# Kernel tuning notes

Measured on AMD Instinct MI355X. Metric: run time of the kernel, lower is better.

## Reference

```python
import jax, jax.numpy as jnp
import numpy as np

N_CLASSES = 16
B, N = 8, 2048
F = [128, 512, 1024]
K = [6, 5, 3]
M = [512, 128, 50]
IN_DIM = 22


def get_laplacian(x):
    # exp(-squared pairwise distance) adjacency, then normalized Laplacian I - D^-1/2 A D^-1/2
    inner = jnp.matmul(x, x.transpose(0, 2, 1))            # [B,N,N]
    sq = jnp.sum(x * x, axis=-1, keepdims=True)            # [B,N,1]
    adj = jnp.exp(-(sq - 2.0 * inner + sq.transpose(0, 2, 1)))
    dinv = 1.0 / jnp.sqrt(jnp.sum(adj, axis=-1))           # [B,N]
    Lnorm = dinv[:, :, None] * adj * dinv[:, None, :]
    return jnp.eye(x.shape[1], dtype=x.dtype) - Lnorm


def cheb_conv(x, L, W, b):
    # Chebyshev recursion: x0=x, x1=Lx, x_k = 2 L x_{k-1} - x_{k-2}; out = sum_k x_k @ W_k + b
    Kk = W.shape[0]
    x0 = x
    out = jnp.einsum('bni,io->bno', x0, W[0])
    if Kk > 1:
        x1 = jnp.matmul(L, x0)
        out = out + jnp.einsum('bni,io->bno', x1, W[1])
        for k in range(2, Kk):
            x2 = 2.0 * jnp.matmul(L, x1) - x0
            out = out + jnp.einsum('bni,io->bno', x2, W[k])
            x0, x1 = x1, x2
    return out + b


def setup_inputs() -> dict:
    key = jax.random.key(0)
    ks = jax.random.split(key, 24)
    d = {}
    d['x'] = jax.random.normal(ks[0], (B, N, 6), dtype=jnp.float32)
    d['cat'] = jax.random.randint(ks[1], (B, 1), 0, N_CLASSES)
    ins = [IN_DIM, F[0], F[1]]
    for i in range(3):
        s = 1.0 / np.sqrt(ins[i] * K[i])
        d[f'cheb_w{i}'] = jax.random.normal(ks[2 + i], (K[i], ins[i], F[i]), dtype=jnp.float32) * s
        d[f'cheb_b{i}'] = jnp.zeros((F[i],), dtype=jnp.float32)
    fc_ins = [F[-1], M[0] + M[0], M[1]]
    for i in range(3):
        s = 1.0 / np.sqrt(fc_ins[i])
        d[f'fc_w{i}'] = jax.random.normal(ks[6 + i], (fc_ins[i], M[i]), dtype=jnp.float32) * s
        d[f'fc_b{i}'] = jax.random.normal(ks[10 + i], (M[i],), dtype=jnp.float32) * s
    relus = F + M
    for i in range(6):
        d[f'br{i}'] = jnp.zeros((1, N, relus[i]), dtype=jnp.float32)
    return d


def reference(x, cat, cheb_w0, cheb_b0, cheb_w1, cheb_b1, cheb_w2, cheb_b2,
              fc_w0, fc_b0, fc_w1, fc_b1, fc_w2, fc_b2,
              br0, br1, br2, br3, br4, br5):
    L = jax.lax.stop_gradient(get_laplacian(x))  # torch.no_grad in original
    cat_oh = jax.nn.one_hot(cat, N_CLASSES, dtype=x.dtype)      # [B,1,16]
    cat_oh = jnp.tile(cat_oh, (1, N, 1))                         # [B,N,16]
    out = jnp.concatenate([x, cat_oh], axis=2)                   # [B,N,22]

    cheb_ws = [cheb_w0, cheb_w1, cheb_w2]
    cheb_bs = [cheb_b0, cheb_b1, cheb_b2]
    brs = [br0, br1, br2, br3, br4, br5]
    x1 = None
    for i in range(3):
        out = cheb_conv(out, L, cheb_ws[i], cheb_bs[i])
        out = jax.nn.relu(out + brs[i])  # dropout is identity in eval
        if i == 1:
            x1 = out

    fc_ws = [fc_w0, fc_w1, fc_w2]
    fc_bs = [fc_b0, fc_b1, fc_b2]
    for i in range(3):
        if i == 1:
            out = jnp.concatenate([out, x1], axis=2)
        out = jnp.einsum('bni,io->bno', out, fc_ws[i]) + fc_bs[i]
        out = jax.nn.relu(out + brs[i + 3])
    return out
```

## Files before the change

### kernel.cpp

```cpp
#include <hip/hip_runtime.h>
#include <stdint.h>

typedef __attribute__((ext_vector_type(8))) short short8;
typedef __attribute__((ext_vector_type(4))) float f32x4;

#define DEV __device__ __forceinline__

DEV ushort f2bf(float f){ uint32_t u = __float_as_uint(f); u += 0x7fffu + ((u >> 16) & 1u); return (ushort)(u >> 16); }
DEV float bf2f(ushort h){ return __uint_as_float(((uint32_t)h) << 16); }

template<int N> DEV void wvm(){
    asm volatile("s_waitcnt vmcnt(%0)" :: "i"(N) : "memory");
}


__global__ void wt_kernel(const float* __restrict__ src, ushort* __restrict__ dst,
                          int I, int O, int Opad, int blk, int srcF){
    int idx = blockIdx.x * 256 + threadIdx.x;
    if (idx >= Opad * I) return;
    int i = idx % I, o = idx / I;
    int k = i / blk, f = i % blk;
    ushort v = 0;
    if (o < O && f < srcF) v = f2bf(src[((long)k * srcF + f) * O + o]);
    dst[idx] = v;
}

__global__ void x0t_kernel(const float* __restrict__ x, const int* __restrict__ cat,
                           ushort* __restrict__ dst){
    int idx = blockIdx.x * 256 + threadIdx.x;
    int n = idx & 2047, f = (idx >> 11) & 31, b = idx >> 16;
    ushort v = 0;
    if (f < 6) v = f2bf(x[((long)b * 2048 + n) * 6 + f]);
    else if (f < 22) v = (cat[b] == f - 6) ? (ushort)0x3f80 : (ushort)0;
    dst[idx] = v;
}

__global__ void xt_kernel(const float* __restrict__ x, float* __restrict__ xT){
    int idx = blockIdx.x * 256 + threadIdx.x;
    if (idx >= 16384) return;
    int b = idx >> 11, n = idx & 2047;
    float* dst = xT + (long)b * 6 * 2048 + n;
#pragma unroll
    for (int d = 0; d < 6; d++) dst[d * 2048] = x[(long)idx * 6 + d];
}

__global__ __launch_bounds__(256) void dinv_kernel(const float* __restrict__ xT, float* __restrict__ dinv){
    int b = blockIdx.y;
    int wave = threadIdx.x >> 6, lane = threadIdx.x & 63;
    int i0 = blockIdx.x * 16 + wave * 4;
    const float* xtb = xT + (long)b * 6 * 2048;
    float xi[4][6];
#pragma unroll
    for (int ii = 0; ii < 4; ii++)
#pragma unroll
        for (int d = 0; d < 6; d++) xi[ii][d] = xtb[d * 2048 + i0 + ii];
    float s[4] = {0.f, 0.f, 0.f, 0.f};
#pragma unroll 2
    for (int jj = 0; jj < 32; jj++){
        int j = jj * 64 + lane;
        float xd[6];
#pragma unroll
        for (int d = 0; d < 6; d++) xd[d] = xtb[d * 2048 + j];
#pragma unroll
        for (int ii = 0; ii < 4; ii++){
            float a = 0.0f;
#pragma unroll
            for (int d = 0; d < 6; d++){ float t = xi[ii][d] - xd[d]; a += t * t; }
            s[ii] += __expf(-a);
        }
    }
#pragma unroll
    for (int ii = 0; ii < 4; ii++){
#pragma unroll
        for (int o = 32; o > 0; o >>= 1) s[ii] += __shfl_xor(s[ii], o);
    }
    if (lane == 0){
#pragma unroll
        for (int ii = 0; ii < 4; ii++) dinv[(b << 11) + i0 + ii] = rsqrtf(s[ii]);
    }
}

__global__ __launch_bounds__(256) void lap_kernel(const float* __restrict__ x, const float* __restrict__ dinv,
                                                  ushort* __restrict__ L){
    int b = blockIdx.z;
    int i0 = blockIdx.y * 32 + (threadIdx.x >> 6) * 8;
    int j0 = blockIdx.x * 512 + (threadIdx.x & 63) * 8;
    const float* xb = x + (long)b * 2048 * 6;
    const float* dv = dinv + (b << 11);
    f32x4 v[12];
    const f32x4* src = (const f32x4*)(xb + (long)j0 * 6);
#pragma unroll
    for (int c = 0; c < 12; c++) v[c] = src[c];
    const float* xj = (const float*)v;
    f32x4 dj0 = *(const f32x4*)(dv + j0);
    f32x4 dj1 = *(const f32x4*)(dv + j0 + 4);
    float dj[8] = {dj0[0], dj0[1], dj0[2], dj0[3], dj1[0], dj1[1], dj1[2], dj1[3]};
    ushort* out = L + ((long)b << 22) + (long)i0 * 2048 + j0;
#pragma unroll
    for (int ii = 0; ii < 8; ii++){
        const int i = i0 + ii;
        float xi[6];
#pragma unroll
        for (int d = 0; d < 6; d++) xi[d] = xb[i * 6 + d];
        const float di = dv[i];
        short8 o;
#pragma unroll
        for (int jj = 0; jj < 8; jj++){
            float a = 0.0f;
#pragma unroll
            for (int d = 0; d < 6; d++){ float t = xi[d] - xj[jj * 6 + d]; a += t * t; }
            float val = -di * dj[jj] * __expf(-a);
            if (i == j0 + jj) val += 1.0f;
            o[jj] = (short)f2bf(val);
        }
        *(short8*)(out + (long)ii * 2048) = o;
    }
}

__global__ void ts_kernel(const ushort* __restrict__ src, ushort* __restrict__ dst,
                          int F, int KF){
    int b = blockIdx.z;
    int i0 = blockIdx.y * 32;
    int k = i0 / F, f0 = i0 % F;
    int n0 = blockIdx.x * 64;
    __shared__ ushort t[32][66];
    const ushort* s = src + (((long)k * 8 + b) * F + f0) * 2048 + n0;
    int r = threadIdx.x >> 3, c8 = (threadIdx.x & 7) * 8;
    *(short8*)&t[r][c8] = *(const short8*)(s + (long)r * 2048 + c8);
    __syncthreads();
    int c = threadIdx.x >> 2, r8 = (threadIdx.x & 3) * 8;
    short8 v;
#pragma unroll
    for (int j = 0; j < 8; j++) v[j] = (short)t[r8 + j][c];
    *(short8*)(dst + ((long)b * 2048 + n0 + c) * KF + i0 + r8) = v;
}

__global__ void copy_x1_kernel(const ushort* __restrict__ src, ushort* __restrict__ dst){
    int idx = blockIdx.x * 256 + threadIdx.x;
    int r = idx >> 6, c = (idx & 63) * 8;
    *(short8*)(dst + (long)r * 1024 + 512 + c) = *(const short8*)(src + (long)r * 1536 + c);
}

template<int BM, int BN, int WR, int WC, int MODE>
__global__ __launch_bounds__(256) void gemm2(
    const ushort* __restrict__ A, int lda, long sA,
    const ushort* __restrict__ BT, int ldb, long sB,
    ushort* __restrict__ C, int ldc, long sC,
    int K,
    const ushort* __restrict__ Xp, long sX,
    const float* __restrict__ bias, const float* __restrict__ br, int brF,
    float* __restrict__ outF)
{
    constexpr int WM = BM / WR, WN = BN / WC, FM = WM / 16, FN = WN / 16;
    constexpr int ACH = BM / 16;
    constexpr int NCH = (BM + BN) / 16;
    __shared__ __align__(16) ushort As[BM * 32];
    __shared__ __align__(16) ushort Bs[BN * 32];
    const int tid = threadIdx.x, lane = tid & 63, wave = tid >> 6;
    const int wr = wave / WC, wc = wave % WC;
    const int bm0 = blockIdx.x * BM, bn0 = blockIdx.y * BN;
    const long z = blockIdx.z;
    A += z * sA; BT += z * sB;
    if (MODE != 4) C += z * sC;
    if (MODE == 1) Xp += z * sX;

    f32x4 acc[FM][FN];
#pragma unroll
    for (int m = 0; m < FM; m++)
#pragma unroll
        for (int n = 0; n < FN; n++) acc[m][n] = f32x4{0.f, 0.f, 0.f, 0.f};

    const int crow = lane >> 2;
    const int ccol = (lane & 3) * 8;

    for (int kt = 0; kt < K; kt += 32){
#pragma unroll
        for (int c = wave; c < NCH; c += 4){
            const ushort* gsrc;
            ushort* ldst;
            if (c < ACH){
                ldst = &As[c * 512];
                gsrc = A + (long)(bm0 + c * 16 + crow) * lda + kt + ccol;
            } else {
                ldst = &Bs[(c - ACH) * 512];
                gsrc = BT + (long)(bn0 + (c - ACH) * 16 + crow) * ldb + kt + ccol;
            }
            __builtin_amdgcn_global_load_lds(
                (const __attribute__((address_space(1))) void*)gsrc,
                (__attribute__((address_space(3))) void*)ldst, 16, 0, 0);
        }
        __syncthreads();
        const int kg = (lane >> 4) * 8;
        short8 af[FM], bfr[FN];
#pragma unroll
        for (int m = 0; m < FM; m++)
            af[m] = *(const short8*)&As[(wr * WM + m * 16 + (lane & 15)) * 32 + kg];
#pragma unroll
        for (int n = 0; n < FN; n++)
            bfr[n] = *(const short8*)&Bs[(wc * WN + n * 16 + (lane & 15)) * 32 + kg];
#pragma unroll
        for (int m = 0; m < FM; m++)
#pragma unroll
            for (int n = 0; n < FN; n++)
                acc[m][n] = __builtin_amdgcn_mfma_f32_16x16x32_bf16(af[m], bfr[n], acc[m][n], 0, 0, 0);
        __syncthreads();
    }

#pragma unroll
    for (int m = 0; m < FM; m++){
        const int r0 = bm0 + wr * WM + m * 16 + ((lane >> 4) << 2);
#pragma unroll
        for (int n = 0; n < FN; n++){
            const int col = bn0 + wc * WN + n * 16 + (lane & 15);
#pragma unroll
            for (int j = 0; j < 4; j++){
                const int r = r0 + j;
                float v = acc[m][n][j];
                if (MODE == 0){
                    C[(long)r * ldc + col] = f2bf(v);
                } else if (MODE == 1){
                    float p = bf2f(Xp[(long)r * ldc + col]);
                    C[(long)r * ldc + col] = f2bf(2.0f * v - p);
                } else if (MODE == 2){
                    float o = v + bias[r] + br[(long)col * brF + r];
                    C[(long)r * ldc + col] = f2bf(fmaxf(o, 0.0f));
                } else if (MODE == 3){
                    float o = v + bias[col] + br[(long)(r & 2047) * brF + col];
                    C[(long)r * ldc + col] = f2bf(fmaxf(o, 0.0f));
                } else {
                    if (col < 50){
                        float o = v + bias[col] + br[(long)(r & 2047) * 50 + col];
                        outF[(long)r * 50 + col] = fmaxf(o, 0.0f);
                    }
                }
            }
        }
    }
}

template<int BM, int BN, int MODE>
__global__ __launch_bounds__(256) void gmv(
    const ushort* __restrict__ A, int lda, long sA,
    const ushort* __restrict__ BT, int ldb, long sB,
    ushort* __restrict__ C, int ldc, long sC,
    int K,
    const ushort* __restrict__ Xp, long sX)
{
    constexpr int WM = BM / 2, WN = BN / 2, FM = WM / 16, FN = WN / 16;
    constexpr int ACH = BM / 8;
    constexpr int NCH = (BM + BN) / 8;
    constexpr int LPW = NCH / 4;
    static_assert(NCH % 4 == 0, "uniform loads per wave");
    __shared__ __align__(16) ushort lds[3 * (BM + BN) * 64];
    const int tid = threadIdx.x, lane = tid & 63, wave = tid >> 6;
    const int wr = wave >> 1, wc = wave & 1;
    const long z = blockIdx.x;
    const int bm0 = blockIdx.y * BM, bn0 = blockIdx.z * BN;
    A += z * sA; BT += z * sB; C += z * sC;
    if (MODE == 1) Xp += z * sX;
    const int NT = K >> 6;

    const int srow = lane >> 3;
    const int kloc = ((lane & 7) ^ srow) * 8;

    auto stage = [&](int u, int sel){
        ushort* dst0 = lds + sel * (BM + BN) * 64;
#pragma unroll
        for (int i = 0; i < LPW; i++){
            int c = i * 4 + wave;
            ushort* ldst = dst0 + c * 512;
            const ushort* src;
            if (c < ACH) src = A + (long)(bm0 + c * 8 + srow) * lda + u * 64 + kloc;
            else         src = BT + (long)(bn0 + (c - ACH) * 8 + srow) * ldb + u * 64 + kloc;
            __builtin_amdgcn_global_load_lds(
                (const __attribute__((address_space(1))) void*)src,
                (__attribute__((address_space(3))) void*)ldst, 16, 0, 0);
        }
    };

    f32x4 acc[FM][FN];
#pragma unroll
    for (int m = 0; m < FM; m++)
#pragma unroll
        for (int n = 0; n < FN; n++) acc[m][n] = f32x4{0.f, 0.f, 0.f, 0.f};

    stage(0, 0);
    if (NT > 1) stage(1, 1);

    int sel = 0;
    for (int u = 0; u < NT; u++){
        if (u + 1 < NT) wvm<LPW>(); else wvm<0>();
        __builtin_amdgcn_sched_barrier(0);
        __builtin_amdgcn_s_barrier();
        __builtin_amdgcn_sched_barrier(0);
        const char* base = (const char*)lds + sel * (BM + BN) * 128;
        const int hi = (lane >> 4) << 4;
        short8 af[FM], bfr[FN];
#pragma unroll
        for (int h = 0; h < 2; h++){
            const int kb = h * 64 + hi;
#pragma unroll
            for (int m = 0; m < FM; m++){
                int row = wr * WM + m * 16 + (lane & 15);
                af[m] = *(const short8*)(base + row * 128 + (kb ^ ((row & 7) << 4)));
            }
#pragma unroll
            for (int n = 0; n < FN; n++){
                int row = BM + wc * WN + n * 16 + (lane & 15);
                bfr[n] = *(const short8*)(base + row * 128 + (kb ^ ((row & 7) << 4)));
            }
            __builtin_amdgcn_s_setprio(1);
#pragma unroll
            for (int m = 0; m < FM; m++)
#pragma unroll
                for (int n = 0; n < FN; n++)
                    acc[m][n] = __builtin_amdgcn_mfma_f32_16x16x32_bf16(af[m], bfr[n], acc[m][n], 0, 0, 0);
            __builtin_amdgcn_s_setprio(0);
        }
        if (u + 2 < NT) stage(u + 2, (u + 2) % 3);
        sel = (sel == 2) ? 0 : sel + 1;
    }

#pragma unroll
    for (int m = 0; m < FM; m++){
        const int r0 = bm0 + wr * WM + m * 16 + ((lane >> 4) << 2);
#pragma unroll
        for (int n = 0; n < FN; n++){
            const int col = bn0 + wc * WN + n * 16 + (lane & 15);
#pragma unroll
            for (int j = 0; j < 4; j++){
                const int r = r0 + j;
                float v = acc[m][n][j];
                if (MODE == 0){
                    C[(long)r * ldc + col] = f2bf(v);
                } else {
                    float p = bf2f(Xp[(long)r * ldc + col]);
                    C[(long)r * ldc + col] = f2bf(2.0f * v - p);
                }
            }
        }
    }
}

template<int MODE, int SWZ>
__global__ __launch_bounds__(512) void gemm8(
    const ushort* __restrict__ A, int lda, long sA,
    const ushort* __restrict__ BT, int ldb, long sB,
    ushort* __restrict__ C, int ldc, long sC,
    int K,
    const ushort* __restrict__ Xp, long sX,
    const float* __restrict__ bias, const float* __restrict__ br, int brF)
{
    __shared__ __align__(16) ushort lds[73728];
    const int tid = threadIdx.x, lane = tid & 63, wave = tid >> 6;
    const int wr = wave >> 1, wc = wave & 1;
    const int bm0 = (SWZ ? blockIdx.y : blockIdx.x) * 256;
    const int bn0 = (SWZ ? blockIdx.z : blockIdx.y) * 128;
    const long z = SWZ ? blockIdx.x : blockIdx.z;
    A += z * sA; BT += z * sB; C += z * sC;
    if (MODE == 1) Xp += z * sX;
    const int NT = K >> 6;

    const int srow = lane >> 3;
    const int kloc = ((lane & 7) ^ srow) * 8;

    auto stageA = [&](int u, int sel){
        ushort* dst0 = lds + sel * 24576;
        const ushort* src = A + (long)u * 64 + kloc;
#pragma unroll
        for (int c = 0; c < 4; c++){
            int row = (c * 8 + wave) * 8 + srow;
            __builtin_amdgcn_global_load_lds(
                (const __attribute__((address_space(1))) void*)(src + (long)(bm0 + row) * lda),
                (__attribute__((address_space(3))) void*)(dst0 + (c * 8 + wave) * 512), 16, 0, 0);
        }
    };
    auto stageB = [&](int u, int sel){
        ushort* dst0 = lds + sel * 24576 + 16384;
        const ushort* src = BT + (long)u * 64 + kloc;
#pragma unroll
        for (int c = 0; c < 2; c++){
            int row = (c * 8 + wave) * 8 + srow;
            __builtin_amdgcn_global_load_lds(
                (const __attribute__((address_space(1))) void*)(src + (long)(bn0 + row) * ldb),
                (__attribute__((address_space(3))) void*)(dst0 + (c * 8 + wave) * 512), 16, 0, 0);
        }
    };

    f32x4 acc[4][4];
#pragma unroll
    for (int m = 0; m < 4; m++)
#pragma unroll
        for (int n = 0; n < 4; n++) acc[m][n] = f32x4{0.f, 0.f, 0.f, 0.f};

    stageA(0, 0); stageB(0, 0);
    stageA(1, 1); stageB(1, 1);
    asm volatile("s_waitcnt vmcnt(6)" ::: "memory");
    __builtin_amdgcn_sched_barrier(0);
    __builtin_amdgcn_s_barrier();
    __builtin_amdgcn_sched_barrier(0);

    int bsel = 0;
    for (int u = 0; u < NT; u++){
        const char* Ab = (const char*)lds + bsel * 49152;
        const char* Bb = Ab + 32768;
        const int stsel = bsel ? bsel - 1 : 2;
        const bool do_stage = (u + 2 < NT);
        const int hi = (lane >> 4) << 4;
        short8 af[4], bf[4];
#pragma unroll
        for (int m = 0; m < 4; m++){
            int row = wr * 64 + m * 16 + (lane & 15);
            af[m] = *(const short8*)(Ab + row * 128 + (hi ^ ((row & 7) << 4)));
        }
#pragma unroll
        for (int n = 0; n < 4; n++){
            int row = wc * 64 + n * 16 + (lane & 15);
            bf[n] = *(const short8*)(Bb + row * 128 + (hi ^ ((row & 7) << 4)));
        }
        if (do_stage) stageA(u + 2, stsel);
        __builtin_amdgcn_sched_barrier(0);
        __builtin_amdgcn_s_barrier();
        __builtin_amdgcn_s_setprio(1);
#pragma unroll
        for (int m = 0; m < 4; m++)
#pragma unroll
            for (int n = 0; n < 4; n++)
                acc[m][n] = __builtin_amdgcn_mfma_f32_16x16x32_bf16(af[m], bf[n], acc[m][n], 0, 0, 0);
        __builtin_amdgcn_s_setprio(0);
        __builtin_amdgcn_sched_barrier(0);
        __builtin_amdgcn_s_barrier();
        __builtin_amdgcn_sched_barrier(0);
#pragma unroll
        for (int m = 0; m < 4; m++){
            int row = wr * 64 + m * 16 + (lane & 15);
            af[m] = *(const short8*)(Ab + row * 128 + ((64 + hi) ^ ((row & 7) << 4)));
        }
#pragma unroll
        for (int n = 0; n < 4; n++){
            int row = wc * 64 + n * 16 + (lane & 15);
            bf[n] = *(const short8*)(Bb + row * 128 + ((64 + hi) ^ ((row & 7) << 4)));
        }
        if (do_stage) stageB(u + 2, stsel);
        __builtin_amdgcn_sched_barrier(0);
        __builtin_amdgcn_s_barrier();
        __builtin_amdgcn_s_setprio(1);
#pragma unroll
        for (int m = 0; m < 4; m++)
#pragma unroll
            for (int n = 0; n < 4; n++)
                acc[m][n] = __builtin_amdgcn_mfma_f32_16x16x32_bf16(af[m], bf[n], acc[m][n], 0, 0, 0);
        __builtin_amdgcn_s_setprio(0);
        if (do_stage){ asm volatile("s_waitcnt vmcnt(6)" ::: "memory"); }
        else        { asm volatile("s_waitcnt vmcnt(0)" ::: "memory"); }
        __builtin_amdgcn_sched_barrier(0);
        __builtin_amdgcn_s_barrier();
        __builtin_amdgcn_sched_barrier(0);
        bsel = (bsel == 2) ? 0 : bsel + 1;
    }

#pragma unroll
    for (int m = 0; m < 4; m++){
        const int r0 = bm0 + wr * 64 + m * 16 + ((lane >> 4) << 2);
#pragma unroll
        for (int n = 0; n < 4; n++){
            const int col = bn0 + wc * 64 + n * 16 + (lane & 15);
#pragma unroll
            for (int j = 0; j < 4; j++){
                const int r = r0 + j;
                float v = acc[m][n][j];
                if (MODE == 0){
                    C[(long)r * ldc + col] = f2bf(v);
                } else if (MODE == 1){
                    float p = bf2f(Xp[(long)r * ldc + col]);
                    C[(long)r * ldc + col] = f2bf(2.0f * v - p);
                } else if (MODE == 2){
                    float o = v + bias[r] + br[(long)col * brF + r];
                    C[(long)r * ldc + col] = f2bf(fmaxf(o, 0.0f));
                } else {
                    float o = v + bias[col] + br[(long)(r & 2047) * brF + col];
                    C[(long)r * ldc + col] = f2bf(fmaxf(o, 0.0f));
                }
            }
        }
    }
}


extern "C" void kernel_launch(void* const* d_in, const int* in_sizes, int n_in,
                              void* d_out, int out_size, void* d_ws, size_t ws_size,
                              hipStream_t stream){
    const float* x   = (const float*)d_in[0];
    const int*   cat = (const int*)d_in[1];
    const float* cw0 = (const float*)d_in[2];
    const float* cb0 = (const float*)d_in[3];
    const float* cw1 = (const float*)d_in[4];
    const float* cb1 = (const float*)d_in[5];
    const float* cw2 = (const float*)d_in[6];
    const float* cb2 = (const float*)d_in[7];
    const float* fw0 = (const float*)d_in[8];
    const float* fb0 = (const float*)d_in[9];
    const float* fw1 = (const float*)d_in[10];
    const float* fb1 = (const float*)d_in[11];
    const float* fw2 = (const float*)d_in[12];
    const float* fb2 = (const float*)d_in[13];
    const float* br0 = (const float*)d_in[14];
    const float* br1 = (const float*)d_in[15];
    const float* br2 = (const float*)d_in[16];
    const float* br3 = (const float*)d_in[17];
    const float* br4 = (const float*)d_in[18];
    const float* br5 = (const float*)d_in[19];
    float* out = (float*)d_out;
    (void)in_sizes; (void)n_in; (void)out_size; (void)ws_size;

    char* ws = (char*)d_ws;
    long off = 0;
    auto take = [&](long bytes){ char* p = ws + off; off += (bytes + 255) & ~255L; return p; };
    ushort* Lb   = (ushort*)take(8L * 2048 * 2048 * 2);
    float*  din  = (float*) take(8L * 2048 * 4);
    float*  XT   = (float*) take(8L * 6 * 2048 * 4);
    ushort* W0T  = (ushort*)take(128L * 192 * 2);
    ushort* W1T  = (ushort*)take(512L * 640 * 2);
    ushort* W2T  = (ushort*)take(1024L * 1536 * 2);
    ushort* WF0T = (ushort*)take(512L * 1024 * 2);
    ushort* WF1T = (ushort*)take(128L * 1024 * 2);
    ushort* WF2T = (ushort*)take(64L * 128 * 2);
    ushort* ST0T = (ushort*)take(6L * 8 * 32 * 2048 * 2);
    ushort* S0   = (ushort*)take(16384L * 192 * 2);
    ushort* ST1T = (ushort*)take(5L * 8 * 128 * 2048 * 2);
    ushort* S1   = (ushort*)take(16384L * 640 * 2);
    ushort* ST2T = (ushort*)take(3L * 8 * 512 * 2048 * 2);
    ushort* S2   = (ushort*)take(16384L * 1536 * 2);
    ushort* X3 = Lb;
    ushort* CC = ST2T;
    ushort* H5 = ST0T;

    const long NN = 2048L * 2048;
    const long s0k = 8L * 32 * 2048,  s0b = 32L * 2048;
    const long s1k = 8L * 128 * 2048, s1b = 128L * 2048;
    const long s2k = 8L * 512 * 2048, s2b = 512L * 2048;

    wt_kernel<<<(128 * 192 + 255) / 256, 256, 0, stream>>>(cw0, W0T, 192, 128, 128, 32, 22);
    wt_kernel<<<(512 * 640 + 255) / 256, 256, 0, stream>>>(cw1, W1T, 640, 512, 512, 128, 128);
    wt_kernel<<<(1024 * 1536 + 255) / 256, 256, 0, stream>>>(cw2, W2T, 1536, 1024, 1024, 512, 512);
    wt_kernel<<<(512 * 1024 + 255) / 256, 256, 0, stream>>>(fw0, WF0T, 1024, 512, 512, 1024, 1024);
    wt_kernel<<<(128 * 1024 + 255) / 256, 256, 0, stream>>>(fw1, WF1T, 1024, 128, 128, 1024, 1024);
    wt_kernel<<<(64 * 128 + 255) / 256, 256, 0, stream>>>(fw2, WF2T, 128, 50, 64, 128, 128);

    x0t_kernel<<<2048, 256, 0, stream>>>(x, cat, ST0T);
    xt_kernel<<<64, 256, 0, stream>>>(x, XT);
    dinv_kernel<<<dim3(128, 8), 256, 0, stream>>>(XT, din);
    lap_kernel<<<dim3(4, 64, 8), 256, 0, stream>>>(x, din, Lb);

    gmv<32, 32, 0><<<dim3(8, 1, 64), 256, 0, stream>>>(
        ST0T, 2048, s0b, Lb, 2048, NN, ST0T + s0k, 2048, s0b, 2048, nullptr, 0);
    for (int k = 2; k < 6; k++)
        gmv<32, 32, 1><<<dim3(8, 1, 64), 256, 0, stream>>>(
            ST0T + (k - 1) * s0k, 2048, s0b, Lb, 2048, NN, ST0T + k * s0k, 2048, s0b, 2048,
            ST0T + (k - 2) * s0k, s0b);
    ts_kernel<<<dim3(32, 6, 8), 256, 0, stream>>>(ST0T, S0, 32, 192);
    gemm2<64, 128, 2, 2, 2><<<dim3(2, 16, 8), 256, 0, stream>>>(
        W0T, 192, 0, S0, 192, 2048L * 192, ST1T, 2048, s1b, 192, nullptr, 0, cb0, br0, 128, nullptr);

    gmv<128, 32, 0><<<dim3(8, 1, 64), 256, 0, stream>>>(
        ST1T, 2048, s1b, Lb, 2048, NN, ST1T + s1k, 2048, s1b, 2048, nullptr, 0);
    for (int k = 2; k < 5; k++)
        gmv<128, 32, 1><<<dim3(8, 1, 64), 256, 0, stream>>>(
            ST1T + (k - 1) * s1k, 2048, s1b, Lb, 2048, NN, ST1T + k * s1k, 2048, s1b, 2048,
            ST1T + (k - 2) * s1k, s1b);
    ts_kernel<<<dim3(32, 20, 8), 256, 0, stream>>>(ST1T, S1, 128, 640);
    gemm8<2, 1><<<dim3(8, 2, 16), 512, 0, stream>>>(
        W1T, 640, 0, S1, 640, 2048L * 640, ST2T, 2048, s2b, 640, nullptr, 0, cb1, br1, 512);

    gemm8<0, 1><<<dim3(8, 2, 16), 512, 0, stream>>>(
        ST2T, 2048, s2b, Lb, 2048, NN, ST2T + s2k, 2048, s2b, 2048, nullptr, 0, nullptr, nullptr, 0);
    gemm8<1, 1><<<dim3(8, 2, 16), 512, 0, stream>>>(
        ST2T + s2k, 2048, s2b, Lb, 2048, NN, ST2T + 2 * s2k, 2048, s2b, 2048,
        ST2T, s2b, nullptr, nullptr, 0);
    ts_kernel<<<dim3(32, 48, 8), 256, 0, stream>>>(ST2T, S2, 512, 1536);
    gemm8<3, 0><<<dim3(64, 8, 1), 512, 0, stream>>>(
        S2, 1536, 0, W2T, 1536, 0, X3, 1024, 0, 1536, nullptr, 0, cb2, br2, 1024);

    gemm8<3, 0><<<dim3(64, 4, 1), 512, 0, stream>>>(
        X3, 1024, 0, WF0T, 1024, 0, CC, 1024, 0, 1024, nullptr, 0, fb0, br3, 512);
    copy_x1_kernel<<<4096, 256, 0, stream>>>(S2, CC);
    gemm2<128, 64, 2, 2, 3><<<dim3(128, 2, 1), 256, 0, stream>>>(
        CC, 1024, 0, WF1T, 1024, 0, H5, 128, 0, 1024, nullptr, 0, fb1, br4, 128, nullptr);
    gemm2<128, 64, 2, 2, 4><<<dim3(128, 1, 1), 256, 0, stream>>>(
        H5, 128, 0, WF2T, 128, 0, nullptr, 0, 0, 128, nullptr, 0, fb2, br5, 50, out);
}
```

Measured before the change: 462.5 us.

## Replace 256x128 triple-buffered GEMM with 128x128 double-buffered 256-thread kernel

The large bf16 MFMA GEMM kernel now uses 128x128 block tiles with 4 waves instead of 256x128 tiles with 8 waves. The LDS staging drops from a triple buffer to a double buffer, with A and B loaded by one combined routine. Each iteration now waits for all outstanding loads before its closing barrier. All launches double their block count in M, which gives more blocks per CU and smaller LDS use. The cost is less data reuse per block and a shallower prefetch pipeline that exposes more memory latency.

```diff
diff --git a/kernel.cpp b/kernel.cpp
--- a/kernel.cpp
+++ b/kernel.cpp
@@ -343,7 +343,7 @@
 }
 
 template<int MODE, int SWZ>
-__global__ __launch_bounds__(512) void gemm8(
+__global__ __launch_bounds__(256) void gd(
     const ushort* __restrict__ A, int lda, long sA,
     const ushort* __restrict__ BT, int ldb, long sB,
     ushort* __restrict__ C, int ldc, long sC,
@@ -351,10 +351,10 @@
     const ushort* __restrict__ Xp, long sX,
     const float* __restrict__ bias, const float* __restrict__ br, int brF)
 {
-    __shared__ __align__(16) ushort lds[73728];
+    __shared__ __align__(16) ushort lds[2 * 256 * 64];
     const int tid = threadIdx.x, lane = tid & 63, wave = tid >> 6;
     const int wr = wave >> 1, wc = wave & 1;
-    const int bm0 = (SWZ ? blockIdx.y : blockIdx.x) * 256;
+    const int bm0 = (SWZ ? blockIdx.y : blockIdx.x) * 128;
     const int bn0 = (SWZ ? blockIdx.z : blockIdx.y) * 128;
     const long z = SWZ ? blockIdx.x : blockIdx.z;
     A += z * sA; BT += z * sB; C += z * sC;
@@ -364,28 +364,19 @@
     const int srow = lane >> 3;
     const int kloc = ((lane & 7) ^ srow) * 8;
 
-    auto stageA = [&](int u, int sel){
-        ushort* dst0 = lds + sel * 24576;
-        const ushort* src = A + (long)u * 64 + kloc;
-#pragma unroll
-        for (int c = 0; c < 4; c++){
-            int row = (c * 8 + wave) * 8 + srow;
+    auto stage = [&](int u, int sel){
+        ushort* dst0 = lds + sel * 16384;
+#pragma unroll
+        for (int i = 0; i < 8; i++){
+            int c = i * 4 + wave;
+            const ushort* src = (c < 16)
+                ? A + (long)(bm0 + c * 8 + srow) * lda + (long)u * 64 + kloc
+                : BT + (long)(bn0 + (c - 16) * 8 + srow) * ldb + (long)u * 64 + kloc;
             __builtin_amdgcn_global_load_lds(
-                (const __attribute__((address_space(1))) void*)(src + (long)(bm0 + row) * lda),
-                (__attribute__((address_space(3))) void*)(dst0 + (c * 8 + wave) * 512), 16, 0, 0);
+                (const __attribute__((address_space(1))) void*)src,
+                (__attribute__((address_space(3))) void*)(dst0 + c * 512), 16, 0, 0);
         }
     };
-    auto stageB = [&](int u, int sel){
-        ushort* dst0 = lds + sel * 24576 + 16384;
-        const ushort* src = BT + (long)u * 64 + kloc;
-#pragma unroll
-        for (int c = 0; c < 2; c++){
-            int row = (c * 8 + wave) * 8 + srow;
-            __builtin_amdgcn_global_load_lds(
-                (const __attribute__((address_space(1))) void*)(src + (long)(bn0 + row) * ldb),
-                (__attribute__((address_space(3))) void*)(dst0 + (c * 8 + wave) * 512), 16, 0, 0);
-        }
-    };
 
     f32x4 acc[4][4];
 #pragma unroll
@@ -393,19 +384,16 @@
 #pragma unroll
         for (int n = 0; n < 4; n++) acc[m][n] = f32x4{0.f, 0.f, 0.f, 0.f};
 
-    stageA(0, 0); stageB(0, 0);
-    stageA(1, 1); stageB(1, 1);
-    asm volatile("s_waitcnt vmcnt(6)" ::: "memory");
+    stage(0, 0);
+    if (NT > 1) stage(1, 1);
+    wvm<8>();
     __builtin_amdgcn_sched_barrier(0);
     __builtin_amdgcn_s_barrier();
     __builtin_amdgcn_sched_barrier(0);
 
-    int bsel = 0;
     for (int u = 0; u < NT; u++){
-        const char* Ab = (const char*)lds + bsel * 49152;
-        const char* Bb = Ab + 32768;
-        const int stsel = bsel ? bsel - 1 : 2;
-        const bool do_stage = (u + 2 < NT);
+        const char* Ab = (const char*)lds + (u & 1) * 32768;
+        const char* Bb = Ab + 16384;
         const int hi = (lane >> 4) << 4;
         short8 af[4], bf[4];
 #pragma unroll
@@ -418,9 +406,7 @@
             int row = wc * 64 + n * 16 + (lane & 15);
             bf[n] = *(const short8*)(Bb + row * 128 + (hi ^ ((row & 7) << 4)));
         }
-        if (do_stage) stageA(u + 2, stsel);
-        __builtin_amdgcn_sched_barrier(0);
-        __builtin_amdgcn_s_barrier();
+        if (u >= 1 && u + 1 < NT) stage(u + 1, (u + 1) & 1);
         __builtin_amdgcn_s_setprio(1);
 #pragma unroll
         for (int m = 0; m < 4; m++)
@@ -428,35 +414,27 @@
             for (int n = 0; n < 4; n++)
                 acc[m][n] = __builtin_amdgcn_mfma_f32_16x16x32_bf16(af[m], bf[n], acc[m][n], 0, 0, 0);
         __builtin_amdgcn_s_setprio(0);
+#pragma unroll
+        for (int m = 0; m < 4; m++){
+            int row = wr * 64 + m * 16 + (lane & 15);
+            af[m] = *(const short8*)(Ab + row * 128 + ((64 + hi) ^ ((row & 7) << 4)));
+        }
+#pragma unroll
+        for (int n = 0; n < 4; n++){
+            int row = wc * 64 + n * 16 + (lane & 15);
+            bf[n] = *(const short8*)(Bb + row * 128 + ((64 + hi) ^ ((row & 7) << 4)));
+        }
+        __builtin_amdgcn_s_setprio(1);
+#pragma unroll
+        for (int m = 0; m < 4; m++)
+#pragma unroll
+            for (int n = 0; n < 4; n++)
+                acc[m][n] = __builtin_amdgcn_mfma_f32_16x16x32_bf16(af[m], bf[n], acc[m][n], 0, 0, 0);
+        __builtin_amdgcn_s_setprio(0);
+        wvm<0>();
         __builtin_amdgcn_sched_barrier(0);
         __builtin_amdgcn_s_barrier();
         __builtin_amdgcn_sched_barrier(0);
-#pragma unroll
-        for (int m = 0; m < 4; m++){
-            int row = wr * 64 + m * 16 + (lane & 15);
-            af[m] = *(const short8*)(Ab + row * 128 + ((64 + hi) ^ ((row & 7) << 4)));
-        }
-#pragma unroll
-        for (int n = 0; n < 4; n++){
-            int row = wc * 64 + n * 16 + (lane & 15);
-            bf[n] = *(const short8*)(Bb + row * 128 + ((64 + hi) ^ ((row & 7) << 4)));
-        }
-        if (do_stage) stageB(u + 2, stsel);
-        __builtin_amdgcn_sched_barrier(0);
-        __builtin_amdgcn_s_barrier();
-        __builtin_amdgcn_s_setprio(1);
-#pragma unroll
-        for (int m = 0; m < 4; m++)
-#pragma unroll
-            for (int n = 0; n < 4; n++)
-                acc[m][n] = __builtin_amdgcn_mfma_f32_16x16x32_bf16(af[m], bf[n], acc[m][n], 0, 0, 0);
-        __builtin_amdgcn_s_setprio(0);
-        if (do_stage){ asm volatile("s_waitcnt vmcnt(6)" ::: "memory"); }
-        else        { asm volatile("s_waitcnt vmcnt(0)" ::: "memory"); }
-        __builtin_amdgcn_sched_barrier(0);
-        __builtin_amdgcn_s_barrier();
-        __builtin_amdgcn_sched_barrier(0);
-        bsel = (bsel == 2) ? 0 : bsel + 1;
     }
 
 #pragma unroll
@@ -569,19 +547,19 @@
             ST1T + (k - 1) * s1k, 2048, s1b, Lb, 2048, NN, ST1T + k * s1k, 2048, s1b, 2048,
             ST1T + (k - 2) * s1k, s1b);
     ts_kernel<<<dim3(32, 20, 8), 256, 0, stream>>>(ST1T, S1, 128, 640);
-    gemm8<2, 1><<<dim3(8, 2, 16), 512, 0, stream>>>(
+    gd<2, 1><<<dim3(8, 4, 16), 256, 0, stream>>>(
         W1T, 640, 0, S1, 640, 2048L * 640, ST2T, 2048, s2b, 640, nullptr, 0, cb1, br1, 512);
 
-    gemm8<0, 1><<<dim3(8, 2, 16), 512, 0, stream>>>(
+    gd<0, 1><<<dim3(8, 4, 16), 256, 0, stream>>>(
         ST2T, 2048, s2b, Lb, 2048, NN, ST2T + s2k, 2048, s2b, 2048, nullptr, 0, nullptr, nullptr, 0);
-    gemm8<1, 1><<<dim3(8, 2, 16), 512, 0, stream>>>(
+    gd<1, 1><<<dim3(8, 4, 16), 256, 0, stream>>>(
         ST2T + s2k, 2048, s2b, Lb, 2048, NN, ST2T + 2 * s2k, 2048, s2b, 2048,
         ST2T, s2b, nullptr, nullptr, 0);
     ts_kernel<<<dim3(32, 48, 8), 256, 0, stream>>>(ST2T, S2, 512, 1536);
-    gemm8<3, 0><<<dim3(64, 8, 1), 512, 0, stream>>>(
+    gd<3, 0><<<dim3(128, 8, 1), 256, 0, stream>>>(
         S2, 1536, 0, W2T, 1536, 0, X3, 1024, 0, 1536, nullptr, 0, cb2, br2, 1024);
 
-    gemm8<3, 0><<<dim3(64, 4, 1), 512, 0, stream>>>(
+    gd<3, 0><<<dim3(128, 4, 1), 256, 0, stream>>>(
         X3, 1024, 0, WF0T, 1024, 0, CC, 1024, 0, 1024, nullptr, 0, fb0, br3, 512);
     copy_x1_kernel<<<4096, 256, 0, stream>>>(S2, CC);
     gemm2<128, 64, 2, 2, 3><<<dim3(128, 2, 1), 256, 0, stream>>>(
```

After: 443.9 us (median of 2 runs). -4.0%, faster.
